# Kernel tuning notes

Measured on AMD Instinct MI355X. Metric: run time of the kernel, lower is better.

The kernel has to match this reference:

```python
import jax, jax.numpy as jnp
import numpy as np

EPS = 1e-7
STRIDE = 1
PAD = 3


def _mantissa_map(v):
    # (|v|+eps) * 2^(-floor(log2(|v|+eps))) - 1  -> mantissa-1 in [0,1)
    a = jnp.abs(v) + EPS
    base = a * jnp.exp2(-jnp.floor(jnp.log2(a))) - 1.0
    # piecewise: >=0.5 -> (1+base)/2, else 1+base  (values in [0.75, 1.5))
    return jnp.where(base >= 0.5, (1.0 + base) * 0.5, 1.0 + base)


def _unfold(x, kH, kW, stride, pad, Ho, Wo):
    # im2col matching torch.nn.Unfold ordering (kernel position index = i*kW + j)
    xp = jnp.pad(x, ((0, 0), (0, 0), (pad, pad), (pad, pad)))
    cols = [xp[:, :, i:i + stride * Ho:stride, j:j + stride * Wo:stride]
            for i in range(kH) for j in range(kW)]
    return jnp.stack(cols, axis=-1)  # (B, C, Ho, Wo, kH*kW)


def setup_inputs() -> dict:
    key = jax.random.key(0)
    k1, k2 = jax.random.split(key)
    x = jax.random.normal(k1, (4, 192, 56, 56), dtype=jnp.float32)
    weight = jax.random.normal(k2, (192, 1, 7, 7), dtype=jnp.float32) * 0.1
    return {"x": x, "weight": weight}


def reference(x, weight):
    B, C, H, W = x.shape
    _, _, kH, kW = weight.shape
    Ho = (H + 2 * PAD - kH) // STRIDE + 1
    Wo = (W + 2 * PAD - kW) // STRIDE + 1
    KK = kH * kW

    # mantissa factors
    m2 = _mantissa_map(weight).reshape(C, KK)[None, :, None, None, :]  # (1,C,1,1,KK)
    m1 = _unfold(_mantissa_map(x), kH, kW, STRIDE, PAD, Ho, Wo)        # (B,C,Ho,Wo,KK)
    # zeros come only from unfold's zero padding; map them to 1 (then 0 after -1)
    m1 = jnp.where(m1 == 0.0, 1.0, m1) - 1.0
    m2 = m2 - 1.0

    factor = (m1 + m2 + 1.0) / ((m1 + 1.0) * (m2 + 1.0))
    factor = jnp.where(jnp.isfinite(factor), factor, 1.0)

    q_x = _unfold(x, kH, kW, STRIDE, PAD, Ho, Wo)          # (B,C,Ho,Wo,KK)
    w = weight.reshape(C, KK)[None, :, None, None, :]       # (1,C,1,1,KK)
    q_y = jnp.sum(factor * (q_x * w), axis=-1)              # (B,C,Ho,Wo)
    return q_y.astype(jnp.float32)
```

## Files before the change

### kernel.cpp

```cpp
#include <hip/hip_runtime.h>

typedef float v2f __attribute__((ext_vector_type(2)));
typedef float v4f __attribute__((ext_vector_type(4)));

#define EPS 1e-7f
#define LDS_ROWS 62
#define LDS_COLS 64

__device__ __forceinline__ float mant_map(float v) {
    float a = fabsf(v) + EPS;
    unsigned int bi = __float_as_uint(a);
    float m = __uint_as_float((bi & 0x007FFFFFu) | 0x3F800000u);
    return (m >= 1.5f) ? 0.5f * m : m;
}

__global__ __launch_bounds__(64) void wprep_kernel(const float* __restrict__ w,
                                                   v2f* __restrict__ wt) {
    int t = blockIdx.x * 64 + threadIdx.x;
    if (t < 192 * 49) {
        float wv = w[t];
        float M2 = mant_map(wv);
        float B = wv / M2;
        wt[t] = (v2f){B, B * (M2 - 1.0f)};
    }
}

__global__ __launch_bounds__(256) void wconv_kernel(const float* __restrict__ x,
                                                    const v2f* __restrict__ wtab,
                                                    float* __restrict__ out) {
    __shared__ v2f sp[LDS_ROWS][LDS_COLS];

    const int lx = threadIdx.x;
    const int ty = threadIdx.y;
    const int tid = ty * 32 + lx;
    const int c = blockIdx.x;
    const int b = blockIdx.y;

    const long plane = (long)(b * 192 + c) * (56 * 56);
    const float* xp = x + plane;
    const v2f* wt = wtab + c * 49;

    for (int idx = tid; idx < LDS_ROWS * LDS_COLS; idx += 256) {
        int r = idx >> 6, lc = idx & 63;
        int ir = r - 3, ic = lc - 3;
        float u = 0.0f;
        if (ir >= 0 && ir < 56 && ic >= 0 && ic < 56)
            u = xp[ir * 56 + ic];
        float v = u * __builtin_amdgcn_rcpf(mant_map(u));
        sp[r][lc] = (v2f){u, v};
    }
    __syncthreads();

    if (lx < 28) {
        const int x0 = lx * 2;
        const int rb = ty * 7;

        v2f a0[7], a1[7];
        #pragma unroll
        for (int r = 0; r < 7; ++r) { a0[r] = (v2f){0.f, 0.f}; a1[r] = (v2f){0.f, 0.f}; }

        #pragma unroll
        for (int ir2 = 0; ir2 < 13; ++ir2) {
            const v4f* q = (const v4f*)&sp[rb + ir2][x0];
            v4f q0 = q[0], q1 = q[1], q2 = q[2], q3 = q[3];
            float t[16] = {q0.x, q0.y, q0.z, q0.w, q1.x, q1.y, q1.z, q1.w,
                           q2.x, q2.y, q2.z, q2.w, q3.x, q3.y, q3.z, q3.w};

            #pragma unroll
            for (int ry = 0; ry < 7; ++ry) {
                const int i = ir2 - ry;
                if (i >= 0 && i <= 6) {
                    const v2f* wr = wt + i * 7;
                    #pragma unroll
                    for (int j = 0; j < 7; ++j) {
                        v2f wc = wr[j];
                        a0[ry] += (v2f){t[2 * j],     t[2 * j + 1]} * wc;
                        a1[ry] += (v2f){t[2 * j + 2], t[2 * j + 3]} * wc;
                    }
                }
            }
        }

        #pragma unroll
        for (int ry = 0; ry < 7; ++ry) {
            float2 o = make_float2(a0[ry].x + a0[ry].y, a1[ry].x + a1[ry].y);
            *(float2*)&out[plane + (rb + ry) * 56 + x0] = o;
        }
    }
}

extern "C" void kernel_launch(void* const* d_in, const int* in_sizes, int n_in,
                              void* d_out, int out_size, void* d_ws, size_t ws_size,
                              hipStream_t stream) {
    const float* x = (const float*)d_in[0];
    const float* w = (const float*)d_in[1];
    float* out = (float*)d_out;
    v2f* wt = (v2f*)d_ws;

    hipLaunchKernelGGL(wprep_kernel, dim3(147), dim3(64), 0, stream, w, wt);
    hipLaunchKernelGGL(wconv_kernel, dim3(192, 4), dim3(32, 8), 0, stream, x, wt, out);
}
```

Baseline: 73.75 us.

## Split each plane into two row halves, fuse weight prep into conv kernel

Removes the separate weight-prep kernel launch by computing the per-channel weight table into shared memory inside the conv kernel. Each channel plane is now split across two blocks of 128 threads (28 output rows each) with a smaller LDS tile, doubling the number of blocks and raising occupancy. Input loads become vectorized float4 reads, with only the halo padding zeroed explicitly. The cost is recomputing the 49-entry weight table in every block and a loaded halo that overlaps between the two blocks of a plane.

After: 69.48 us. -5.8%, faster.

```diff
diff --git a/kernel.cpp b/kernel.cpp
--- a/kernel.cpp
+++ b/kernel.cpp
@@ -4,8 +4,6 @@
 typedef float v4f __attribute__((ext_vector_type(4)));
 
 #define EPS 1e-7f
-#define LDS_ROWS 62
-#define LDS_COLS 64
 
 __device__ __forceinline__ float mant_map(float v) {
     float a = fabsf(v) + EPS;
@@ -14,40 +12,50 @@
     return (m >= 1.5f) ? 0.5f * m : m;
 }
 
-__global__ __launch_bounds__(64) void wprep_kernel(const float* __restrict__ w,
-                                                   v2f* __restrict__ wt) {
-    int t = blockIdx.x * 64 + threadIdx.x;
-    if (t < 192 * 49) {
-        float wv = w[t];
-        float M2 = mant_map(wv);
-        float B = wv / M2;
-        wt[t] = (v2f){B, B * (M2 - 1.0f)};
-    }
-}
-
-__global__ __launch_bounds__(256) void wconv_kernel(const float* __restrict__ x,
-                                                    const v2f* __restrict__ wtab,
-                                                    float* __restrict__ out) {
-    __shared__ v2f sp[LDS_ROWS][LDS_COLS];
+__global__ __launch_bounds__(128, 3) void wconv_kernel(const float* __restrict__ x,
+                                                       const float* __restrict__ w,
+                                                       float* __restrict__ out) {
+    __shared__ v2f sp[34][64];
+    __shared__ v2f swt[49];
 
     const int lx = threadIdx.x;
     const int ty = threadIdx.y;
     const int tid = ty * 32 + lx;
     const int c = blockIdx.x;
     const int b = blockIdx.y;
+    const int tz = blockIdx.z;
 
-    const long plane = (long)(b * 192 + c) * (56 * 56);
+    const int y0 = 28 * tz;
+    const int g0 = (tz == 0) ? 0 : 25;
+    const int l0 = (tz == 0) ? 3 : 0;
+    const int z0 = (tz == 0) ? 0 : 31;
+
+    const long plane = (long)(b * 192 + c) * 3136;
     const float* xp = x + plane;
-    const v2f* wt = wtab + c * 49;
 
-    for (int idx = tid; idx < LDS_ROWS * LDS_COLS; idx += 256) {
-        int r = idx >> 6, lc = idx & 63;
-        int ir = r - 3, ic = lc - 3;
-        float u = 0.0f;
-        if (ir >= 0 && ir < 56 && ic >= 0 && ic < 56)
-            u = xp[ir * 56 + ic];
-        float v = u * __builtin_amdgcn_rcpf(mant_map(u));
-        sp[r][lc] = (v2f){u, v};
+    if (tid < 49) {
+        float wv = w[c * 49 + tid];
+        float M2 = mant_map(wv);
+        float B = wv / M2;
+        swt[tid] = (v2f){B, B * (M2 - 1.0f)};
+    }
+
+    for (int t = tid; t < 192; t += 128)
+        ((v2f*)sp)[z0 * 64 + t] = (v2f){0.f, 0.f};
+    for (int t = tid; t < 248; t += 128) {
+        int r = l0 + (t >> 3), k = t & 7;
+        int col = (k < 3) ? k : 56 + k;
+        sp[r][col] = (v2f){0.f, 0.f};
+    }
+
+    for (int t = tid; t < 434; t += 128) {
+        int r = t / 14, q4 = t % 14;
+        v4f u4 = *(const v4f*)(xp + (g0 + r) * 56 + q4 * 4);
+        v2f* dst = &sp[l0 + r][3 + q4 * 4];
+        dst[0] = (v2f){u4.x, u4.x * __builtin_amdgcn_rcpf(mant_map(u4.x))};
+        dst[1] = (v2f){u4.y, u4.y * __builtin_amdgcn_rcpf(mant_map(u4.y))};
+        dst[2] = (v2f){u4.z, u4.z * __builtin_amdgcn_rcpf(mant_map(u4.z))};
+        dst[3] = (v2f){u4.w, u4.w * __builtin_amdgcn_rcpf(mant_map(u4.w))};
     }
     __syncthreads();
 
@@ -60,22 +68,20 @@
         for (int r = 0; r < 7; ++r) { a0[r] = (v2f){0.f, 0.f}; a1[r] = (v2f){0.f, 0.f}; }
 
         #pragma unroll
-        for (int ir2 = 0; ir2 < 13; ++ir2) {
-            const v4f* q = (const v4f*)&sp[rb + ir2][x0];
+        for (int ir = 0; ir < 13; ++ir) {
+            const v4f* q = (const v4f*)&sp[rb + ir][x0];
             v4f q0 = q[0], q1 = q[1], q2 = q[2], q3 = q[3];
-            float t[16] = {q0.x, q0.y, q0.z, q0.w, q1.x, q1.y, q1.z, q1.w,
-                           q2.x, q2.y, q2.z, q2.w, q3.x, q3.y, q3.z, q3.w};
-
+            v2f p[8] = {{q0.x, q0.y}, {q0.z, q0.w}, {q1.x, q1.y}, {q1.z, q1.w},
+                        {q2.x, q2.y}, {q2.z, q2.w}, {q3.x, q3.y}, {q3.z, q3.w}};
             #pragma unroll
             for (int ry = 0; ry < 7; ++ry) {
-                const int i = ir2 - ry;
+                const int i = ir - ry;
                 if (i >= 0 && i <= 6) {
-                    const v2f* wr = wt + i * 7;
                     #pragma unroll
                     for (int j = 0; j < 7; ++j) {
-                        v2f wc = wr[j];
-                        a0[ry] += (v2f){t[2 * j],     t[2 * j + 1]} * wc;
-                        a1[ry] += (v2f){t[2 * j + 2], t[2 * j + 3]} * wc;
+                        v2f wc = swt[i * 7 + j];
+                        a0[ry] += p[j] * wc;
+                        a1[ry] += p[j + 1] * wc;
                     }
                 }
             }
@@ -84,7 +90,7 @@
         #pragma unroll
         for (int ry = 0; ry < 7; ++ry) {
             float2 o = make_float2(a0[ry].x + a0[ry].y, a1[ry].x + a1[ry].y);
-            *(float2*)&out[plane + (rb + ry) * 56 + x0] = o;
+            *(float2*)&out[plane + (y0 + rb + ry) * 56 + x0] = o;
         }
     }
 }
@@ -95,8 +101,6 @@
     const float* x = (const float*)d_in[0];
     const float* w = (const float*)d_in[1];
     float* out = (float*)d_out;
-    v2f* wt = (v2f*)d_ws;
 
-    hipLaunchKernelGGL(wprep_kernel, dim3(147), dim3(64), 0, stream, w, wt);
-    hipLaunchKernelGGL(wconv_kernel, dim3(192, 4), dim3(32, 8), 0, stream, x, wt, out);
+    hipLaunchKernelGGL(wconv_kernel, dim3(192, 4, 2), dim3(32, 4), 0, stream, x, w, out);
 }
```
